# Performance work log

Hardware: AMD Instinct MI355X
Metric: run time of the kernel (lower is better)

The kernel has to match this reference:

```python
import jax, jax.numpy as jnp
import numpy as np

GLM_HIDDEN = 256
K = 3
REL_NUM = K + 1
NUM_BASES = 2
BATCH = 8
SLEN = 2048


def setup_inputs() -> dict:
    key = jax.random.key(0)
    k1, k2, k3, k4, k5 = jax.random.split(key, 5)
    D = GLM_HIDDEN
    x = jax.random.normal(k1, (BATCH, SLEN, D), dtype=jnp.float32)
    # RGCNConv basis decomposition params: W_r = sum_b comp[r,b] * basis[b]
    scale = 1.0 / np.sqrt(D)
    basis = jax.random.normal(k2, (NUM_BASES, D, D), dtype=jnp.float32) * scale
    comp = jax.random.normal(k3, (REL_NUM, NUM_BASES), dtype=jnp.float32)
    root = jax.random.normal(k4, (D, D), dtype=jnp.float32) * scale
    bias = jax.random.normal(k5, (D,), dtype=jnp.float32) * 0.01
    return {"x": x, "comp": comp, "basis": basis, "root": root, "bias": bias}


def reference(x, comp, basis, root, bias):
    B, S, D = x.shape
    R = comp.shape[0]
    Kthr = R - 1
    idx = jnp.arange(S)
    # edge (source s -> target t) has relation min(|t+1 - s|, K); full S x S edge set
    rel = jnp.minimum(jnp.abs((idx[None, :] + 1) - idx[:, None]), Kthr)  # [S(source), S(target)]
    masks = (rel[None, :, :] == jnp.arange(R)[:, None, None]).astype(x.dtype)  # [R,S,T]
    deg = masks.sum(axis=1)  # [R,T] in-degree per relation (PyG aggr='mean')
    inv_deg = jnp.where(deg > 0, 1.0 / deg, 0.0)
    A = masks * inv_deg[:, None, :]  # normalized adjacency per relation [R,S,T]
    # basis-decomposed relation weights
    W = jnp.einsum('rb,bio->rio', comp, basis)  # [R,D,D]
    # aggregate then transform: out[b,t] = sum_r (mean_{s in N_r(t)} x[b,s]) @ W_r
    agg = jnp.einsum('rst,bsi->brti', A, x)  # [B,R,S,D]
    out = jnp.einsum('brti,rio->bto', agg, W)
    out = out + jnp.einsum('bsi,io->bso', x, root) + bias
    return out
```

## Files before the change

kernel.cpp:

```cpp
#include <hip/hip_runtime.h>

#define D 256
#define S 2048
#define B 8
#define DSQ (D * D)
#define INV3 (1.0f / 2043.0f)

typedef __bf16 bf16x8 __attribute__((ext_vector_type(8)));
typedef float f32x4 __attribute__((ext_vector_type(4)));

__device__ __forceinline__ unsigned short f2bf(float f) {
    union { float f; unsigned int u; } v; v.f = f;
    unsigned int u = v.u;
    u += 0x7fffu + ((u >> 16) & 1u);
    return (unsigned short)(u >> 16);
}

__device__ __forceinline__ void gl2lds16(const void* g, void* l) {
    __builtin_amdgcn_global_load_lds(
        (const __attribute__((address_space(1))) void*)g,
        (__attribute__((address_space(3))) void*)l, 16, 0, 0);
}

__global__ __launch_bounds__(256) void k_prep(const float* __restrict__ x,
                                              const float* __restrict__ comp,
                                              const float* __restrict__ basis,
                                              const float* __restrict__ root,
                                              unsigned short* __restrict__ xh,
                                              float* __restrict__ part,
                                              unsigned short* __restrict__ Cbs) {
    int blk = blockIdx.x;
    int tid = threadIdx.x;
    int b = blk >> 6, chunk = blk & 63;
    __shared__ float ps[4][D];
    int rg = tid >> 6;
    int c4 = (tid & 63) << 2;
    int row0 = chunk * 32 + rg * 8;
    const float4* xb = (const float4*)(x + ((size_t)b * S + row0) * D + c4);
    ushort4* dst = (ushort4*)(xh + ((size_t)(1 + b * S + row0)) * D + c4);
    float4 s = {0.f, 0.f, 0.f, 0.f};
    #pragma unroll
    for (int i = 0; i < 8; ++i) {
        float4 v = xb[(size_t)i * 64];
        ushort4 o;
        o.x = f2bf(v.x); o.y = f2bf(v.y); o.z = f2bf(v.z); o.w = f2bf(v.w);
        dst[(size_t)i * 64] = o;
        s.x += v.x; s.y += v.y; s.z += v.z; s.w += v.w;
    }
    *(float4*)&ps[rg][c4] = s;

    if (blk < 160) {
        int step = blk >> 2, q = blk & 3;
        int ji = step >> 3, kc = step & 7;
        int n = tid;
        float a0 = (ji == 2) ? 1.f : 0.f;
        float a1 = (ji == 1 || ji == 3) ? 0.5f : 0.f;
        float a2 = (ji == 0 || ji == 4) ? 0.5f : 0.f;
        float ar = (ji == 1) ? 1.f : 0.f;
        float cb0 = a0 * comp[0] + a1 * comp[2] + a2 * comp[4] - INV3 * comp[6];
        float cb1 = a0 * comp[1] + a1 * comp[3] + a2 * comp[5] - INV3 * comp[7];
        unsigned short buf[8];
        #pragma unroll
        for (int kk = 0; kk < 8; ++kk) {
            int i = kc * 32 + q * 8 + kk;
            buf[kk] = f2bf(cb0 * basis[i * D + n] + cb1 * basis[DSQ + i * D + n]
                           + ar * root[i * D + n]);
        }
        *(uint4*)(Cbs + ((size_t)step * 256 + n) * 32 + q * 8) = *(uint4*)buf;
    }
    __syncthreads();
    if (tid < 64)
        *(float4*)&part[(size_t)blk * D + tid * 4] =
            *(float4*)&ps[0][tid * 4] + *(float4*)&ps[1][tid * 4] +
            *(float4*)&ps[2][tid * 4] + *(float4*)&ps[3][tid * 4];
}

__global__ __launch_bounds__(256) void k_weights(
        const float* __restrict__ basis, const float* __restrict__ comp,
        const float* __restrict__ root, const float* __restrict__ bias,
        const float* __restrict__ part, const float* __restrict__ x,
        float* __restrict__ Tb, float* __restrict__ out) {
    int blk = blockIdx.x;
    int tid = threadIdx.x;

    if (blk < 8) {
        int b = blk;
        __shared__ float tot[D];
        float t = 0.f;
        #pragma unroll 8
        for (int c = 0; c < 64; ++c) t += part[(size_t)(b * 64 + c) * D + tid];
        tot[tid] = t;
        __syncthreads();
        int o = tid;
        float c30 = comp[6], c31 = comp[7];
        float acc = 0.f;
        #pragma unroll 4
        for (int k = 0; k < D; ++k)
            acc += tot[k] * (c30 * basis[k * D + o] + c31 * basis[DSQ + k * D + o]);
        Tb[b * D + o] = bias[o] + acc * INV3;
    } else {
        int r = blk - 8;
        const int tl[4] = {0, S - 3, S - 2, S - 1};
        int t = tl[r & 3], b = r >> 2;
        __shared__ float z0[D], z1[D], xr[D];
        const float* xb = x + (size_t)b * S * D;
        int i = tid;
        float tot = 0.f;
        #pragma unroll 8
        for (int c = 0; c < 64; ++c) tot += part[(size_t)(b * 64 + c) * D + i];
        float x_t = xb[(size_t)t * D + i];
        float v0 = (t + 1 < S) ? xb[(size_t)(t + 1) * D + i] : 0.f;
        float d1 = 1.f + ((t + 2 < S) ? 1.f : 0.f);
        float v1 = (x_t + ((t + 2 < S) ? xb[(size_t)(t + 2) * D + i] : 0.f)) / d1;
        float s2 = ((t - 1 >= 0) ? xb[(size_t)(t - 1) * D + i] : 0.f)
                 + ((t + 3 < S) ? xb[(size_t)(t + 3) * D + i] : 0.f);
        int d2i = ((t - 1 >= 0) ? 1 : 0) + ((t + 3 < S) ? 1 : 0);
        float v2 = d2i ? s2 / (float)d2i : 0.f;
        float wsum = 0.f;
        for (int s = t - 1; s <= t + 3; ++s)
            if (s >= 0 && s < S) wsum += xb[(size_t)s * D + i];
        int d3i = ((t - 1 > 0) ? (t - 1) : 0) + ((S - 4 - t > 0) ? (S - 4 - t) : 0);
        float v3 = d3i ? (tot - wsum) / (float)d3i : 0.f;
        z0[i] = comp[0] * v0 + comp[2] * v1 + comp[4] * v2 + comp[6] * v3;
        z1[i] = comp[1] * v0 + comp[3] * v1 + comp[5] * v2 + comp[7] * v3;
        xr[i] = x_t;
        __syncthreads();
        int o = tid;
        float acc = 0.f;
        #pragma unroll 8
        for (int k = 0; k < D; ++k)
            acc += z0[k] * basis[k * D + o] + z1[k] * basis[DSQ + k * D + o]
                 + xr[k] * root[k * D + o];
        out[(((size_t)b * S + t) << 8) + o] = acc + bias[o];
    }
}

__global__ __launch_bounds__(256) void k_bulk(
        const unsigned short* __restrict__ xh,
        const unsigned short* __restrict__ Cbs,
        const float* __restrict__ Tb,
        float* __restrict__ out) {
    __shared__ __align__(16) unsigned short xs[132 * 256];
    const int tid  = threadIdx.x;
    const int lane = tid & 63;
    const int w    = tid >> 6;
    const int wm   = w & 1;
    const int wn   = w >> 1;
    const int mblk = blockIdx.x;
    const int nblk = blockIdx.y;
    const int b  = mblk >> 4;
    const int t0 = (mblk & 15) << 7;
    const size_t rowbase = (size_t)b * S + t0;

    #pragma unroll
    for (int q = 0; q < 16; ++q) {
        int F = (q * 256 + tid) * 16;
        int r = F >> 9;
        int c16 = (F >> 4) & 31;
        int gc = (c16 & 24) | ((c16 ^ r) & 7);
        gl2lds16((const char*)xh + ((rowbase + r) << 9) + (gc << 4), (char*)xs + F);
    }
    if (tid < 128) {
        int F = (4096 + tid) * 16;
        int r = F >> 9;
        int c16 = (F >> 4) & 31;
        int gc = (c16 & 24) | ((c16 ^ r) & 7);
        gl2lds16((const char*)xh + ((rowbase + r) << 9) + (gc << 4), (char*)xs + F);
    }
    __syncthreads();

    const int rlo = lane & 15, q4 = lane >> 4;
    const int nstrip = nblk * 128 + wn * 64;
    const int mbase  = wm * 64;

    #define BFRAG(st, nt) (*(const bf16x8*)(Cbs + \
        (((size_t)(st) * 256 + nstrip + (nt) * 16 + rlo) << 5) + (q4 << 3)))
    #define AFRAG(st, mt) (*(const bf16x8*)((const char*)xs + \
        (((mbase + (mt) * 16 + rlo + ((st) >> 3))) << 9) + \
        (((((st) & 7) * 4 + q4) & 24 | ((((st) & 7) * 4 + q4) ^ \
          (mbase + (mt) * 16 + rlo + ((st) >> 3))) & 7) << 4)))

    f32x4 acc[4][4] = {};
    bf16x8 bb[4][4];
    bf16x8 aa[2][4];
    #pragma unroll
    for (int nt = 0; nt < 4; ++nt) {
        bb[0][nt] = BFRAG(0, nt); bb[1][nt] = BFRAG(1, nt); bb[2][nt] = BFRAG(2, nt);
    }
    #pragma unroll
    for (int mt = 0; mt < 4; ++mt) aa[0][mt] = AFRAG(0, mt);

    #pragma unroll
    for (int step = 0; step < 40; ++step) {
        const int pfB = (step + 3 < 40) ? step + 3 : 39;
        #pragma unroll
        for (int nt = 0; nt < 4; ++nt) bb[(step + 3) & 3][nt] = BFRAG(pfB, nt);
        const int pfA = (step + 1 < 40) ? step + 1 : 39;
        #pragma unroll
        for (int mt = 0; mt < 4; ++mt) aa[(step + 1) & 1][mt] = AFRAG(pfA, mt);

        #pragma unroll
        for (int mt = 0; mt < 4; ++mt)
            #pragma unroll
            for (int nt = 0; nt < 4; ++nt)
                acc[mt][nt] = __builtin_amdgcn_mfma_f32_16x16x32_bf16(
                    aa[step & 1][mt], bb[step & 3][nt], acc[mt][nt], 0, 0, 0);
    }
    #undef BFRAG
    #undef AFRAG

    const int col = lane & 15, rq = (lane >> 4) << 2;
    #pragma unroll
    for (int nt = 0; nt < 4; ++nt) {
        int n = nstrip + nt * 16 + col;
        float tb = Tb[b * D + n];
        #pragma unroll
        for (int mt = 0; mt < 4; ++mt) {
            #pragma unroll
            for (int i = 0; i < 4; ++i) {
                int t = t0 + mbase + mt * 16 + rq + i;
                if (t >= 1 && t <= S - 4)
                    out[(((size_t)b * S + t) << 8) + n] = acc[mt][nt][i] + tb;
            }
        }
    }
}


extern "C" void kernel_launch(void* const* d_in, const int* in_sizes, int n_in,
                              void* d_out, int out_size, void* d_ws, size_t ws_size,
                              hipStream_t stream) {
    const float* x     = (const float*)d_in[0];
    const float* comp  = (const float*)d_in[1];
    const float* basis = (const float*)d_in[2];
    const float* root  = (const float*)d_in[3];
    const float* bias  = (const float*)d_in[4];
    float* out = (float*)d_out;

    char* ws = (char*)d_ws;
    float* part         = (float*)(ws);
    float* Tb           = (float*)(ws + 524288);
    unsigned short* Cbs = (unsigned short*)(ws + 532480);
    unsigned short* xh  = (unsigned short*)(ws + 1187840);

    k_prep   <<<512,          256, 0, stream>>>(x, comp, basis, root, xh, part, Cbs);
    k_weights<<<40,           256, 0, stream>>>(basis, comp, root, bias, part, x, Tb, out);
    k_bulk   <<<dim3(128, 2), 256, 0, stream>>>(xh, Cbs, Tb, out);
}
```

Before: 118.9 us.

## Fuse weights/boundary kernel into bulk GEMM kernel to drop a launch

Removes the separate k_weights launch. Each bulk GEMM block now sums the per-batch partials, computes its half of the relation-3 bias term for its 128 output columns, and the blocks covering the first and last time tiles also compute the four boundary rows. This saves a kernel launch and the intermediate Tb buffer round trip. In exchange, every block redundantly reduces the partials and does a 256x128 GEMV from global basis memory, and the edge blocks take on extra serial boundary work.

```diff
diff --git a/kernel.cpp b/kernel.cpp
--- a/kernel.cpp
+++ b/kernel.cpp
@@ -75,81 +75,28 @@
             *(float4*)&ps[2][tid * 4] + *(float4*)&ps[3][tid * 4];
 }
 
-__global__ __launch_bounds__(256) void k_weights(
-        const float* __restrict__ basis, const float* __restrict__ comp,
-        const float* __restrict__ root, const float* __restrict__ bias,
-        const float* __restrict__ part, const float* __restrict__ x,
-        float* __restrict__ Tb, float* __restrict__ out) {
-    int blk = blockIdx.x;
-    int tid = threadIdx.x;
-
-    if (blk < 8) {
-        int b = blk;
-        __shared__ float tot[D];
-        float t = 0.f;
-        #pragma unroll 8
-        for (int c = 0; c < 64; ++c) t += part[(size_t)(b * 64 + c) * D + tid];
-        tot[tid] = t;
-        __syncthreads();
-        int o = tid;
-        float c30 = comp[6], c31 = comp[7];
-        float acc = 0.f;
-        #pragma unroll 4
-        for (int k = 0; k < D; ++k)
-            acc += tot[k] * (c30 * basis[k * D + o] + c31 * basis[DSQ + k * D + o]);
-        Tb[b * D + o] = bias[o] + acc * INV3;
-    } else {
-        int r = blk - 8;
-        const int tl[4] = {0, S - 3, S - 2, S - 1};
-        int t = tl[r & 3], b = r >> 2;
-        __shared__ float z0[D], z1[D], xr[D];
-        const float* xb = x + (size_t)b * S * D;
-        int i = tid;
-        float tot = 0.f;
-        #pragma unroll 8
-        for (int c = 0; c < 64; ++c) tot += part[(size_t)(b * 64 + c) * D + i];
-        float x_t = xb[(size_t)t * D + i];
-        float v0 = (t + 1 < S) ? xb[(size_t)(t + 1) * D + i] : 0.f;
-        float d1 = 1.f + ((t + 2 < S) ? 1.f : 0.f);
-        float v1 = (x_t + ((t + 2 < S) ? xb[(size_t)(t + 2) * D + i] : 0.f)) / d1;
-        float s2 = ((t - 1 >= 0) ? xb[(size_t)(t - 1) * D + i] : 0.f)
-                 + ((t + 3 < S) ? xb[(size_t)(t + 3) * D + i] : 0.f);
-        int d2i = ((t - 1 >= 0) ? 1 : 0) + ((t + 3 < S) ? 1 : 0);
-        float v2 = d2i ? s2 / (float)d2i : 0.f;
-        float wsum = 0.f;
-        for (int s = t - 1; s <= t + 3; ++s)
-            if (s >= 0 && s < S) wsum += xb[(size_t)s * D + i];
-        int d3i = ((t - 1 > 0) ? (t - 1) : 0) + ((S - 4 - t > 0) ? (S - 4 - t) : 0);
-        float v3 = d3i ? (tot - wsum) / (float)d3i : 0.f;
-        z0[i] = comp[0] * v0 + comp[2] * v1 + comp[4] * v2 + comp[6] * v3;
-        z1[i] = comp[1] * v0 + comp[3] * v1 + comp[5] * v2 + comp[7] * v3;
-        xr[i] = x_t;
-        __syncthreads();
-        int o = tid;
-        float acc = 0.f;
-        #pragma unroll 8
-        for (int k = 0; k < D; ++k)
-            acc += z0[k] * basis[k * D + o] + z1[k] * basis[DSQ + k * D + o]
-                 + xr[k] * root[k * D + o];
-        out[(((size_t)b * S + t) << 8) + o] = acc + bias[o];
-    }
-}
-
-__global__ __launch_bounds__(256) void k_bulk(
+__global__ __launch_bounds__(256) void k_main(
         const unsigned short* __restrict__ xh,
         const unsigned short* __restrict__ Cbs,
-        const float* __restrict__ Tb,
+        const float* __restrict__ part,
+        const float* __restrict__ x,
+        const float* __restrict__ comp, const float* __restrict__ basis,
+        const float* __restrict__ root, const float* __restrict__ bias,
         float* __restrict__ out) {
     __shared__ __align__(16) unsigned short xs[132 * 256];
+    __shared__ float tot[D];
+    __shared__ float tbp[2][128];
+    __shared__ float z0[D], z1[D], xr[D], bp[128];
     const int tid  = threadIdx.x;
     const int lane = tid & 63;
     const int w    = tid >> 6;
     const int wm   = w & 1;
     const int wn   = w >> 1;
-    const int mblk = blockIdx.x;
-    const int nblk = blockIdx.y;
-    const int b  = mblk >> 4;
-    const int t0 = (mblk & 15) << 7;
+    const int blk  = blockIdx.x;
+    const int nblk = blk & 1;
+    const int mblk = (blk >> 1) & 15;
+    const int b    = blk >> 5;
+    const int t0   = mblk << 7;
     const size_t rowbase = (size_t)b * S + t0;
 
     #pragma unroll
@@ -209,11 +156,35 @@
     #undef BFRAG
     #undef AFRAG
 
+    {
+        float s = 0.f;
+        const float* pp = part + (size_t)b * 64 * D + tid;
+        #pragma unroll 8
+        for (int c = 0; c < 64; ++c) s += pp[(size_t)c * D];
+        tot[tid] = s;
+    }
+    __syncthreads();
+
+    {
+        int o = nblk * 128 + (tid & 127);
+        int kh = tid >> 7;
+        float c6 = comp[6], c7 = comp[7];
+        float a = 0.f;
+        #pragma unroll 4
+        for (int kk = 0; kk < 128; ++kk) {
+            int k = kh * 128 + kk;
+            a += tot[k] * (c6 * basis[k * D + o] + c7 * basis[DSQ + k * D + o]);
+        }
+        tbp[kh][tid & 127] = a;
+    }
+    __syncthreads();
+
     const int col = lane & 15, rq = (lane >> 4) << 2;
     #pragma unroll
     for (int nt = 0; nt < 4; ++nt) {
-        int n = nstrip + nt * 16 + col;
-        float tb = Tb[b * D + n];
+        int nloc = wn * 64 + nt * 16 + col;
+        int n = nblk * 128 + nloc;
+        float tb = bias[n] + INV3 * (tbp[0][nloc] + tbp[1][nloc]);
         #pragma unroll
         for (int mt = 0; mt < 4; ++mt) {
             #pragma unroll
@@ -222,6 +193,49 @@
                 if (t >= 1 && t <= S - 4)
                     out[(((size_t)b * S + t) << 8) + n] = acc[mt][nt][i] + tb;
             }
+        }
+    }
+
+    if (mblk != 0 && mblk != 15) return;
+    const int ntb = (mblk == 0) ? 1 : 3;
+    const float* xb = x + (size_t)b * S * D;
+    for (int bi = 0; bi < ntb; ++bi) {
+        int t = (mblk == 0) ? 0 : (S - 3 + bi);
+        {
+            int i = tid;
+            float x_t = xb[(size_t)t * D + i];
+            float v0 = (t + 1 < S) ? xb[(size_t)(t + 1) * D + i] : 0.f;
+            float d1 = 1.f + ((t + 2 < S) ? 1.f : 0.f);
+            float v1 = (x_t + ((t + 2 < S) ? xb[(size_t)(t + 2) * D + i] : 0.f)) / d1;
+            float s2 = ((t - 1 >= 0) ? xb[(size_t)(t - 1) * D + i] : 0.f)
+                     + ((t + 3 < S) ? xb[(size_t)(t + 3) * D + i] : 0.f);
+            int d2i = ((t - 1 >= 0) ? 1 : 0) + ((t + 3 < S) ? 1 : 0);
+            float v2 = d2i ? s2 / (float)d2i : 0.f;
+            float wsum = 0.f;
+            for (int s = t - 1; s <= t + 3; ++s)
+                if (s >= 0 && s < S) wsum += xb[(size_t)s * D + i];
+            int d3i = ((t - 1 > 0) ? (t - 1) : 0) + ((S - 4 - t > 0) ? (S - 4 - t) : 0);
+            float v3 = d3i ? (tot[i] - wsum) / (float)d3i : 0.f;
+            __syncthreads();
+            z0[i] = comp[0] * v0 + comp[2] * v1 + comp[4] * v2 + comp[6] * v3;
+            z1[i] = comp[1] * v0 + comp[3] * v1 + comp[5] * v2 + comp[7] * v3;
+            xr[i] = x_t;
+        }
+        __syncthreads();
+        {
+            int o = nblk * 128 + (tid & 127);
+            int kh = tid >> 7;
+            float a = 0.f;
+            #pragma unroll 4
+            for (int kk = 0; kk < 128; ++kk) {
+                int k = kh * 128 + kk;
+                a += z0[k] * basis[k * D + o] + z1[k] * basis[DSQ + k * D + o]
+                   + xr[k] * root[k * D + o];
+            }
+            if (kh) bp[tid & 127] = a;
+            __syncthreads();
+            if (!kh)
+                out[(((size_t)b * S + t) << 8) + o] = a + bp[tid & 127] + bias[o];
         }
     }
 }
@@ -239,11 +253,9 @@
 
     char* ws = (char*)d_ws;
     float* part         = (float*)(ws);
-    float* Tb           = (float*)(ws + 524288);
-    unsigned short* Cbs = (unsigned short*)(ws + 532480);
-    unsigned short* xh  = (unsigned short*)(ws + 1187840);
-
-    k_prep   <<<512,          256, 0, stream>>>(x, comp, basis, root, xh, part, Cbs);
-    k_weights<<<40,           256, 0, stream>>>(basis, comp, root, bias, part, x, Tb, out);
-    k_bulk   <<<dim3(128, 2), 256, 0, stream>>>(xh, Cbs, Tb, out);
-}
+    unsigned short* Cbs = (unsigned short*)(ws + 524288);
+    unsigned short* xh  = (unsigned short*)(ws + 1179648);
+
+    k_prep<<<512, 256, 0, stream>>>(x, comp, basis, root, xh, part, Cbs);
+    k_main<<<256, 256, 0, stream>>>(xh, Cbs, part, x, comp, basis, root, bias, out);
+}
```

After: 135.3 us. 13.8% more time.
